# Performance work log

Hardware: AMD Instinct MI355X
Metric: run time of the kernel (lower is better)

Reference implementation:

```python
import jax, jax.numpy as jnp
import numpy as np

B, S, E, H = 4, 2048, 1024, 16
D = E // H  # head_dim = 64


def setup_inputs() -> dict:
    key = jax.random.key(0)
    ks = jax.random.split(key, 5)
    return {
        "x": jax.random.normal(ks[0], (B, S, E), dtype=jnp.float32),
        "w_qkv": jax.random.normal(ks[1], (3 * E, E), dtype=jnp.float32) * (E ** -0.5),
        "b_qkv": jax.random.normal(ks[2], (3 * E,), dtype=jnp.float32) * 0.02,
        "w_proj": jax.random.normal(ks[3], (E, E), dtype=jnp.float32) * (E ** -0.5),
        "b_proj": jax.random.normal(ks[4], (E,), dtype=jnp.float32) * 0.02,
    }


def reference(x, w_qkv, b_qkv, w_proj, b_proj):
    # fused QKV projection: [B,S,E] -> [B,S,3E] -> [B,S,3,H,D]
    qkv = (jnp.einsum("bse,fe->bsf", x, w_qkv) + b_qkv).reshape(B, S, 3, H, D)
    q, k, v = qkv[:, :, 0], qkv[:, :, 1], qkv[:, :, 2]  # each [B,S,H,D]
    scale = 1.0 / jnp.sqrt(jnp.asarray(D, dtype=q.dtype))
    scores = jnp.einsum("bqhd,bkhd->bhqk", q, k) * scale  # [B,H,S,S]
    attn = jax.nn.softmax(scores, axis=-1)
    out = jnp.einsum("bhqk,bkhd->bqhd", attn, v).reshape(B, S, E)
    return jnp.einsum("bse,fe->bsf", out, w_proj) + b_proj
```

## Files before the change

kernel.cpp:

```cpp
#include <hip/hip_runtime.h>
#include <cstdint>
#include <cstddef>

#define B_ 4
#define S_ 2048
#define E_ 1024
#define H_ 16
#define D_ 64
#define M_ (B_*S_)
#define NE_ ((size_t)B_*H_*S_*D_)

typedef unsigned int  u32;
typedef unsigned short u16;
typedef __attribute__((ext_vector_type(8))) short bf16x8;
typedef __attribute__((ext_vector_type(4))) float f32x4;
typedef __attribute__((ext_vector_type(2))) unsigned int u32x2;

__device__ __forceinline__ u16 f2bf(float x) {
    u32 u = __float_as_uint(x);
    u32 r = (u + 0x7FFFu + ((u >> 16) & 1u)) >> 16;
    return (u16)r;
}
__device__ __forceinline__ float bf2f(u16 h) { return __uint_as_float((u32)h << 16); }

__device__ __forceinline__ u32 cvtpk_bf16(float lo, float hi) {
    u32 r;
    asm("v_cvt_pk_bf16_f32 %0, %1, %2" : "=v"(r) : "v"(lo), "v"(hi));
    return r;
}

__device__ __forceinline__ void gload_lds16(const void* gsrc, void* lds) {
    __builtin_amdgcn_global_load_lds(
        (const __attribute__((address_space(1))) u32*)gsrc,
        (__attribute__((address_space(3))) u32*)lds, 16, 0, 0);
}


__global__ __launch_bounds__(256)
void convert_img(const float* __restrict__ src, u16* __restrict__ dh, u16* __restrict__ dl)
{
    const int tile = blockIdx.x;
    const int nt = tile >> 4, kt = tile & 15;
    const size_t tb = (size_t)tile << 12;
    #pragma unroll
    for (int u = 0; u < 2; ++u) {
        const int ci = threadIdx.x + u * 256;
        const int r  = ci >> 3;
        const int c  = ci & 7;
        const float* s = src + ((size_t)(nt * 64 + r)) * 1024 + kt * 64 + c * 8;
        const float4 f0 = *(const float4*)s;
        const float4 f1 = *(const float4*)(s + 4);
        const float vals[8] = {f0.x, f0.y, f0.z, f0.w, f1.x, f1.y, f1.z, f1.w};
        __align__(16) short hs[8];
        __align__(16) short ls[8];
        #pragma unroll
        for (int j = 0; j < 8; ++j) {
            const u16 h = f2bf(vals[j]);
            hs[j] = (short)h;
            ls[j] = (short)f2bf(vals[j] - bf2f(h));
        }
        const size_t eoff = tb + r * 64 + ((size_t)(c ^ (r & 7)) << 3);
        *(bf16x8*)(dh + eoff) = *(const bf16x8*)hs;
        *(bf16x8*)(dl + eoff) = *(const bf16x8*)ls;
    }
}

template<int MODE>
__global__ __launch_bounds__(256)
void gemm_mfma(const u16* __restrict__ AIh, const u16* __restrict__ AIl,
               const u16* __restrict__ BIh, const u16* __restrict__ BIl,
               const float* __restrict__ bias, float* __restrict__ Cout,
               u16* __restrict__ qh, u16* __restrict__ ql,
               u16* __restrict__ kh,
               u16* __restrict__ vh, u16* __restrict__ vl)
{
    __shared__ __align__(16) u16 sA[2][2][4096];
    __shared__ __align__(16) u16 sB[2][2][4096];

    const int tid = threadIdx.x, lane = tid & 63, w = tid >> 6;
    const int quad = lane >> 4, l15 = lane & 15;
    const int m0  = blockIdx.x * 128;
    const int n0  = blockIdx.y * 128;
    const int mt0 = blockIdx.x * 2;
    const int nt0 = blockIdx.y * 2;
    const int rw  = w >> 1;
    const int cw  = w & 1;

    const int isB = w >> 1;
    const int sbw = w & 1;

    f32x4 acc[4][4];
    #pragma unroll
    for (int i = 0; i < 4; ++i)
        #pragma unroll
        for (int j = 0; j < 4; ++j)
            acc[i][j] = (f32x4){0.f, 0.f, 0.f, 0.f};

    for (int kt = 0; kt < 16; ++kt) {
        __syncthreads();
        {
            const size_t atile = ((size_t)((mt0 + sbw) * 16 + kt)) << 12;
            const size_t btile = ((size_t)((nt0 + sbw) * 16 + kt)) << 12;
            const u16* srcH = isB ? (BIh + btile) : (AIh + atile);
            const u16* srcL = isB ? (BIl + btile) : (AIl + atile);
            u16* dstH = isB ? &sB[sbw][0][0] : &sA[sbw][0][0];
            u16* dstL = isB ? &sB[sbw][1][0] : &sA[sbw][1][0];
            #pragma unroll
            for (int it = 0; it < 8; ++it)
                gload_lds16(srcH + it * 512 + lane * 8, dstH + it * 512);
            #pragma unroll
            for (int it = 0; it < 8; ++it)
                gload_lds16(srcL + it * 512 + lane * 8, dstL + it * 512);
        }
        __syncthreads();

        #pragma unroll
        for (int kk = 0; kk < 2; ++kk) {
            bf16x8 aH[4], aL[4], bH[4], bL[4];
            #pragma unroll
            for (int i = 0; i < 4; ++i) {
                const int r = i * 16 + l15;
                const int off = r * 64 + (((kk * 4 + quad) ^ (r & 7)) << 3);
                aH[i] = *(const bf16x8*)&sA[rw][0][off];
                aL[i] = *(const bf16x8*)&sA[rw][1][off];
            }
            #pragma unroll
            for (int j = 0; j < 4; ++j) {
                const int r = j * 16 + l15;
                const int off = r * 64 + (((kk * 4 + quad) ^ (r & 7)) << 3);
                bH[j] = *(const bf16x8*)&sB[cw][0][off];
                bL[j] = *(const bf16x8*)&sB[cw][1][off];
            }
            #pragma unroll
            for (int i = 0; i < 4; ++i)
                #pragma unroll
                for (int j = 0; j < 4; ++j) {
                    acc[i][j] = __builtin_amdgcn_mfma_f32_16x16x32_bf16(aL[i], bH[j], acc[i][j], 0, 0, 0);
                    acc[i][j] = __builtin_amdgcn_mfma_f32_16x16x32_bf16(aH[i], bL[j], acc[i][j], 0, 0, 0);
                    acc[i][j] = __builtin_amdgcn_mfma_f32_16x16x32_bf16(aH[i], bH[j], acc[i][j], 0, 0, 0);
                }
        }
    }

    const int fbase = n0 + cw * 64;
    float bj[4];
    #pragma unroll
    for (int j = 0; j < 4; ++j) bj[j] = bias[fbase + j * 16 + l15];

    if (MODE == 0) {
        const int cR = fbase >> 10;
        const int hh = (fbase >> 6) & 15;
        #pragma unroll
        for (int i = 0; i < 4; ++i)
            #pragma unroll
            for (int j = 0; j < 4; ++j)
                #pragma unroll
                for (int reg = 0; reg < 4; ++reg) {
                    float val = acc[i][j][reg] + bj[j];
                    const int m = m0 + rw * 64 + i * 16 + quad * 4 + reg;
                    const int d = j * 16 + l15;
                    const int bb = m >> 11, s = m & 2047;
                    const int bh = bb * 16 + hh;
                    if (cR == 0) val *= 0.18033688011112042f;
                    const u16 h = f2bf(val);
                    if (cR == 0) {
                        const u16 lo = f2bf(val - bf2f(h));
                        const size_t idx = ((size_t)bh * 2048 + s) * 64 + d;
                        qh[idx] = h; ql[idx] = lo;
                    } else if (cR == 1) {
                        const size_t tile = (size_t)bh * 32 + (s >> 6);
                        const int r = s & 63;
                        const size_t off = (tile << 12) + r * 64 + (((d >> 3) ^ (r & 7)) << 3) + (d & 7);
                        kh[off] = h;
                    } else {
                        const u16 lo = f2bf(val - bf2f(h));
                        const size_t tile = (size_t)bh * 32 + (s >> 6);
                        const size_t off = (tile << 12) + d * 64 + ((((s & 63) >> 3) ^ (d & 7)) << 3) + (s & 7);
                        vh[off] = h; vl[off] = lo;
                    }
                }
    } else {
        #pragma unroll
        for (int i = 0; i < 4; ++i)
            #pragma unroll
            for (int j = 0; j < 4; ++j)
                #pragma unroll
                for (int reg = 0; reg < 4; ++reg) {
                    const int m = m0 + rw * 64 + i * 16 + quad * 4 + reg;
                    const int f = fbase + j * 16 + l15;
                    Cout[(size_t)m * 1024 + f] = acc[i][j][reg] + bj[j];
                }
    }
}

__global__ __launch_bounds__(256, 3)
void attn_mfma(const u16* __restrict__ qh, const u16* __restrict__ ql,
               const u16* __restrict__ kh,
               const u16* __restrict__ vh, const u16* __restrict__ vl,
               u16* __restrict__ oh, u16* __restrict__ ol)
{
    __shared__ __align__(16) u16 KV[3][4096];

    const int tid  = threadIdx.x;
    const int lane = tid & 63, w = tid >> 6;
    const int quad = lane >> 4, l15 = lane & 15;
    const int bh = blockIdx.y;
    const int q0 = blockIdx.x * 128 + w * 32;

    bf16x8 Qf[2][2][2];
    #pragma unroll
    for (int qs = 0; qs < 2; ++qs)
        #pragma unroll
        for (int kk = 0; kk < 2; ++kk) {
            const size_t idx = ((size_t)bh * S_ + q0 + qs * 16 + l15) * 64 + kk * 32 + quad * 8;
            Qf[qs][kk][0] = *(const bf16x8*)(qh + idx);
            Qf[qs][kk][1] = *(const bf16x8*)(ql + idx);
        }

    f32x4 O[2][4];
    float l_part[2] = {0.f, 0.f};
    #pragma unroll
    for (int qs = 0; qs < 2; ++qs)
        #pragma unroll
        for (int ds = 0; ds < 4; ++ds)
            O[qs][ds] = (f32x4){0.f, 0.f, 0.f, 0.f};

    const char* gk[3] = {(const char*)kh, (const char*)vh, (const char*)vl};

    for (int kt = 0; kt < S_ / 64; ++kt) {
        __syncthreads();
        const size_t tb = (((size_t)bh * 32 + kt) << 13);
        #pragma unroll
        for (int a = 0; a < 3; ++a)
            #pragma unroll
            for (int it = 0; it < 2; ++it) {
                const int off = w * 2048 + it * 1024;
                gload_lds16(gk[a] + tb + off + lane * 16, (char*)&KV[a][0] + off);
            }
        __syncthreads();

        f32x4 S[2][4];
        #pragma unroll
        for (int qs = 0; qs < 2; ++qs)
            #pragma unroll
            for (int ks = 0; ks < 4; ++ks)
                S[qs][ks] = (f32x4){-23.083120654223414f, -23.083120654223414f,
                                    -23.083120654223414f, -23.083120654223414f};

        __builtin_amdgcn_s_setprio(1);
        #pragma unroll
        for (int ks = 0; ks < 4; ++ks) {
            const int r = ks * 16 + l15;
            #pragma unroll
            for (int kk = 0; kk < 2; ++kk) {
                const int c = (kk * 4 + quad) ^ (r & 7);
                const bf16x8 Kh = *(const bf16x8*)&KV[0][r * 64 + c * 8];
                #pragma unroll
                for (int qs = 0; qs < 2; ++qs) {
                    S[qs][ks] = __builtin_amdgcn_mfma_f32_16x16x32_bf16(Kh, Qf[qs][kk][1], S[qs][ks], 0, 0, 0);
                    S[qs][ks] = __builtin_amdgcn_mfma_f32_16x16x32_bf16(Kh, Qf[qs][kk][0], S[qs][ks], 0, 0, 0);
                }
            }
        }
        __builtin_amdgcn_s_setprio(0);

        u32 PA[2][2][4];
        #pragma unroll
        for (int qs = 0; qs < 2; ++qs) {
            float lsum = 0.f;
            u32 PK[4][2];
            #pragma unroll
            for (int ks = 0; ks < 4; ++ks) {
                const float p0 = __builtin_exp2f(S[qs][ks][0]);
                const float p1 = __builtin_exp2f(S[qs][ks][1]);
                const float p2 = __builtin_exp2f(S[qs][ks][2]);
                const float p3 = __builtin_exp2f(S[qs][ks][3]);
                lsum += (p0 + p1) + (p2 + p3);
                PK[ks][0] = cvtpk_bf16(p0, p1);
                PK[ks][1] = cvtpk_bf16(p2, p3);
            }
            l_part[qs] += lsum;
            #pragma unroll
            for (int kk = 0; kk < 2; ++kk) {
                const u32x2 t0 = __builtin_amdgcn_permlane32_swap(PK[2 * kk][0], PK[2 * kk + 1][0], false, false);
                const u32x2 w02 = __builtin_amdgcn_permlane16_swap(t0.x, t0.y, false, false);
                const u32x2 t1 = __builtin_amdgcn_permlane32_swap(PK[2 * kk][1], PK[2 * kk + 1][1], false, false);
                const u32x2 w13 = __builtin_amdgcn_permlane16_swap(t1.x, t1.y, false, false);
                PA[qs][kk][0] = w02.x;
                PA[qs][kk][1] = w13.x;
                PA[qs][kk][2] = w02.y;
                PA[qs][kk][3] = w13.y;
            }
        }

        __builtin_amdgcn_s_setprio(1);
        #pragma unroll
        for (int kk = 0; kk < 2; ++kk) {
            union { u32 w4[4]; bf16x8 v; } pu0, pu1;
            #pragma unroll
            for (int c = 0; c < 4; ++c) { pu0.w4[c] = PA[0][kk][c]; pu1.w4[c] = PA[1][kk][c]; }
            const bf16x8 paf[2] = {pu0.v, pu1.v};
            #pragma unroll
            for (int ds = 0; ds < 4; ++ds) {
                const int r = ds * 16 + l15;
                const int c = (kk * 4 + quad) ^ (r & 7);
                const bf16x8 Vh = *(const bf16x8*)&KV[1][r * 64 + c * 8];
                const bf16x8 Vl = *(const bf16x8*)&KV[2][r * 64 + c * 8];
                #pragma unroll
                for (int qs = 0; qs < 2; ++qs) {
                    O[qs][ds] = __builtin_amdgcn_mfma_f32_16x16x32_bf16(Vl, paf[qs], O[qs][ds], 0, 0, 0);
                    O[qs][ds] = __builtin_amdgcn_mfma_f32_16x16x32_bf16(Vh, paf[qs], O[qs][ds], 0, 0, 0);
                }
            }
        }
        __builtin_amdgcn_s_setprio(0);
    }

    float linv[2];
    #pragma unroll
    for (int qs = 0; qs < 2; ++qs) {
        float rs = l_part[qs];
        rs += __shfl_xor(rs, 16);
        rs += __shfl_xor(rs, 32);
        linv[qs] = 1.f / rs;
    }

    const int bb = bh >> 4, hh = bh & 15;
    #pragma unroll
    for (int qs = 0; qs < 2; ++qs) {
        const float inv = linv[qs];
        const int s = q0 + qs * 16 + l15;
        const int m = bb * 2048 + s;
        const int mt = m >> 6, r = m & 63;
        const size_t tbase = ((size_t)(mt * 16 + hh)) << 12;
        #pragma unroll
        for (int ds = 0; ds < 4; ++ds) {
            const int d0 = ds * 16 + quad * 4;
            const float v0 = O[qs][ds][0] * inv;
            const float v1 = O[qs][ds][1] * inv;
            const float v2 = O[qs][ds][2] * inv;
            const float v3 = O[qs][ds][3] * inv;
            const u32 h01 = cvtpk_bf16(v0, v1);
            const u32 h23 = cvtpk_bf16(v2, v3);
            const float r0 = v0 - bf2f((u16)h01);
            const float r1 = v1 - bf2f((u16)(h01 >> 16));
            const float r2 = v2 - bf2f((u16)h23);
            const float r3 = v3 - bf2f((u16)(h23 >> 16));
            const u32 l01 = cvtpk_bf16(r0, r1);
            const u32 l23 = cvtpk_bf16(r2, r3);
            const size_t off = tbase + r * 64 + (size_t)((((d0 >> 3) ^ (r & 7)) << 3) + (d0 & 7));
            *(u32x2*)(oh + off) = (u32x2){h01, h23};
            *(u32x2*)(ol + off) = (u32x2){l01, l23};
        }
    }
}

extern "C" void kernel_launch(void* const* d_in, const int* in_sizes, int n_in,
                              void* d_out, int out_size, void* d_ws, size_t ws_size,
                              hipStream_t stream) {
    const float* x      = (const float*)d_in[0];
    const float* w_qkv  = (const float*)d_in[1];
    const float* b_qkv  = (const float*)d_in[2];
    const float* w_proj = (const float*)d_in[3];
    const float* b_proj = (const float*)d_in[4];
    float* out = (float*)d_out;

    u16* qh  = (u16*)d_ws;
    u16* ql  = qh + NE_;
    u16* kh  = ql + NE_;
    u16* vh  = kh + NE_;
    u16* vl  = vh + NE_;
    u16* xh  = vl + NE_;
    u16* xl  = xh + NE_;
    u16* wqh = xl + NE_;
    u16* wql = wqh + (size_t)3 * 1024 * 1024;
    u16* oh  = xh;
    u16* ol  = xl;
    u16* wph = wqh;
    u16* wpl = wph + (size_t)1024 * 1024;

    convert_img<<<(M_ / 64) * 16, 256, 0, stream>>>(x, xh, xl);
    convert_img<<<48 * 16, 256, 0, stream>>>(w_qkv, wqh, wql);

    {
        dim3 grid(M_ / 128, (3 * E_) / 128);
        gemm_mfma<0><<<grid, 256, 0, stream>>>(xh, xl, wqh, wql,
                                               b_qkv, nullptr, qh, ql, kh, vh, vl);
    }
    {
        dim3 grid(S_ / 128, B_ * H_);
        attn_mfma<<<grid, 256, 0, stream>>>(qh, ql, kh, vh, vl, oh, ol);
    }
    convert_img<<<16 * 16, 256, 0, stream>>>(w_proj, wph, wpl);
    {
        dim3 grid(M_ / 128, E_ / 128);
        gemm_mfma<1><<<grid, 256, 0, stream>>>(oh, ol, wph, wpl,
                                               b_proj, out, nullptr, nullptr, nullptr,
                                               nullptr, nullptr);
    }
}
```

Baseline: 438.9 us.

## Double-buffer GEMM LDS tiles with 32-wide K image layout and 256x128 blocks

Re-lays out the bf16 hi/lo image tiles as 64x32 K-slices with a new XOR swizzle, in convert_img and in the attention output writer. The GEMM now uses 512-thread blocks covering 256x128, a double-buffered LDS ring, and a prefetch of the next K-slice issued before the MFMAs, with one barrier per iteration and raised wave priority around the MFMA block. This is meant to hide global-to-LDS latency and increase B-tile reuse, at the cost of more LDS per block and a need for all layout producers and consumers to stay consistent.

```diff
diff --git a/kernel.cpp b/kernel.cpp
--- a/kernel.cpp
+++ b/kernel.cpp
@@ -40,33 +40,32 @@
 void convert_img(const float* __restrict__ src, u16* __restrict__ dh, u16* __restrict__ dl)
 {
     const int tile = blockIdx.x;
-    const int nt = tile >> 4, kt = tile & 15;
-    const size_t tb = (size_t)tile << 12;
-    #pragma unroll
-    for (int u = 0; u < 2; ++u) {
-        const int ci = threadIdx.x + u * 256;
-        const int r  = ci >> 3;
-        const int c  = ci & 7;
-        const float* s = src + ((size_t)(nt * 64 + r)) * 1024 + kt * 64 + c * 8;
-        const float4 f0 = *(const float4*)s;
-        const float4 f1 = *(const float4*)(s + 4);
-        const float vals[8] = {f0.x, f0.y, f0.z, f0.w, f1.x, f1.y, f1.z, f1.w};
-        __align__(16) short hs[8];
-        __align__(16) short ls[8];
-        #pragma unroll
-        for (int j = 0; j < 8; ++j) {
-            const u16 h = f2bf(vals[j]);
-            hs[j] = (short)h;
-            ls[j] = (short)f2bf(vals[j] - bf2f(h));
-        }
-        const size_t eoff = tb + r * 64 + ((size_t)(c ^ (r & 7)) << 3);
-        *(bf16x8*)(dh + eoff) = *(const bf16x8*)hs;
-        *(bf16x8*)(dl + eoff) = *(const bf16x8*)ls;
-    }
+    const int rt = tile >> 5, kt = tile & 31;
+    const size_t tb = (size_t)tile * 2048;
+    const int ci = threadIdx.x;
+    const int l  = ci >> 3;
+    const int ph = ci & 7;
+    const int s  = ph ^ (l & 7);
+    const int r  = (l << 1) | (s >> 2);
+    const int k0 = (s & 3) << 3;
+    const float* sp = src + ((size_t)(rt * 64 + r)) * 1024 + kt * 32 + k0;
+    const float4 f0 = *(const float4*)sp;
+    const float4 f1 = *(const float4*)(sp + 4);
+    const float vals[8] = {f0.x, f0.y, f0.z, f0.w, f1.x, f1.y, f1.z, f1.w};
+    __align__(16) short hs[8];
+    __align__(16) short ls[8];
+    #pragma unroll
+    for (int j = 0; j < 8; ++j) {
+        const u16 h = f2bf(vals[j]);
+        hs[j] = (short)h;
+        ls[j] = (short)f2bf(vals[j] - bf2f(h));
+    }
+    *(bf16x8*)(dh + tb + ci * 8) = *(const bf16x8*)hs;
+    *(bf16x8*)(dl + tb + ci * 8) = *(const bf16x8*)ls;
 }
 
 template<int MODE>
-__global__ __launch_bounds__(256)
+__global__ __launch_bounds__(512, 2)
 void gemm_mfma(const u16* __restrict__ AIh, const u16* __restrict__ AIl,
                const u16* __restrict__ BIh, const u16* __restrict__ BIl,
                const float* __restrict__ bias, float* __restrict__ Cout,
@@ -74,20 +73,26 @@
                u16* __restrict__ kh,
                u16* __restrict__ vh, u16* __restrict__ vl)
 {
-    __shared__ __align__(16) u16 sA[2][2][4096];
-    __shared__ __align__(16) u16 sB[2][2][4096];
+    __shared__ __align__(16) u16 sT[2][12][2048];
 
     const int tid = threadIdx.x, lane = tid & 63, w = tid >> 6;
     const int quad = lane >> 4, l15 = lane & 15;
-    const int m0  = blockIdx.x * 128;
+    const int m0  = blockIdx.x * 256;
     const int n0  = blockIdx.y * 128;
-    const int mt0 = blockIdx.x * 2;
+    const int mt0 = blockIdx.x * 4;
     const int nt0 = blockIdx.y * 2;
     const int rw  = w >> 1;
     const int cw  = w & 1;
 
-    const int isB = w >> 1;
-    const int sbw = w & 1;
+    const u16* srcq[6];
+    #pragma unroll
+    for (int it = 0; it < 6; ++it) {
+        const int g = w * 6 + it;
+        const int t = g >> 2, qtr = g & 3;
+        const u16* img = (t < 4) ? AIh : (t < 8) ? AIl : (t < 10) ? BIh : BIl;
+        const int rtile = (t < 8) ? (mt0 + (t & 3)) : (nt0 + (t & 1));
+        srcq[it] = img + (size_t)rtile * (32 * 2048) + qtr * 512 + lane * 8;
+    }
 
     f32x4 acc[4][4];
     #pragma unroll
@@ -96,50 +101,46 @@
         for (int j = 0; j < 4; ++j)
             acc[i][j] = (f32x4){0.f, 0.f, 0.f, 0.f};
 
-    for (int kt = 0; kt < 16; ++kt) {
+    #pragma unroll
+    for (int it = 0; it < 6; ++it)
+        gload_lds16(srcq[it], (char*)&sT[0][0][0] + (w * 6 + it) * 1024);
+    __syncthreads();
+
+    #pragma unroll 2
+    for (int kt = 0; kt < 32; ++kt) {
+        const int cur = kt & 1;
+        bf16x8 aH[4], aL[4], bH[4], bL[4];
+        #pragma unroll
+        for (int i = 0; i < 4; ++i) {
+            const int r = i * 16 + l15, l = r >> 1;
+            const int off = l * 64 + (((((r & 1) << 2) + quad) ^ (l & 7)) << 3);
+            aH[i] = *(const bf16x8*)&sT[cur][rw][off];
+            aL[i] = *(const bf16x8*)&sT[cur][4 + rw][off];
+        }
+        #pragma unroll
+        for (int j = 0; j < 4; ++j) {
+            const int r = j * 16 + l15, l = r >> 1;
+            const int off = l * 64 + (((((r & 1) << 2) + quad) ^ (l & 7)) << 3);
+            bH[j] = *(const bf16x8*)&sT[cur][8 + cw][off];
+            bL[j] = *(const bf16x8*)&sT[cur][10 + cw][off];
+        }
+        if (kt < 31) {
+            #pragma unroll
+            for (int it = 0; it < 6; ++it)
+                gload_lds16(srcq[it] + (size_t)(kt + 1) * 2048,
+                            (char*)&sT[cur ^ 1][0][0] + (w * 6 + it) * 1024);
+        }
+        __builtin_amdgcn_s_setprio(1);
+        #pragma unroll
+        for (int i = 0; i < 4; ++i)
+            #pragma unroll
+            for (int j = 0; j < 4; ++j) {
+                acc[i][j] = __builtin_amdgcn_mfma_f32_16x16x32_bf16(aL[i], bH[j], acc[i][j], 0, 0, 0);
+                acc[i][j] = __builtin_amdgcn_mfma_f32_16x16x32_bf16(aH[i], bL[j], acc[i][j], 0, 0, 0);
+                acc[i][j] = __builtin_amdgcn_mfma_f32_16x16x32_bf16(aH[i], bH[j], acc[i][j], 0, 0, 0);
+            }
+        __builtin_amdgcn_s_setprio(0);
         __syncthreads();
-        {
-            const size_t atile = ((size_t)((mt0 + sbw) * 16 + kt)) << 12;
-            const size_t btile = ((size_t)((nt0 + sbw) * 16 + kt)) << 12;
-            const u16* srcH = isB ? (BIh + btile) : (AIh + atile);
-            const u16* srcL = isB ? (BIl + btile) : (AIl + atile);
-            u16* dstH = isB ? &sB[sbw][0][0] : &sA[sbw][0][0];
-            u16* dstL = isB ? &sB[sbw][1][0] : &sA[sbw][1][0];
-            #pragma unroll
-            for (int it = 0; it < 8; ++it)
-                gload_lds16(srcH + it * 512 + lane * 8, dstH + it * 512);
-            #pragma unroll
-            for (int it = 0; it < 8; ++it)
-                gload_lds16(srcL + it * 512 + lane * 8, dstL + it * 512);
-        }
-        __syncthreads();
-
-        #pragma unroll
-        for (int kk = 0; kk < 2; ++kk) {
-            bf16x8 aH[4], aL[4], bH[4], bL[4];
-            #pragma unroll
-            for (int i = 0; i < 4; ++i) {
-                const int r = i * 16 + l15;
-                const int off = r * 64 + (((kk * 4 + quad) ^ (r & 7)) << 3);
-                aH[i] = *(const bf16x8*)&sA[rw][0][off];
-                aL[i] = *(const bf16x8*)&sA[rw][1][off];
-            }
-            #pragma unroll
-            for (int j = 0; j < 4; ++j) {
-                const int r = j * 16 + l15;
-                const int off = r * 64 + (((kk * 4 + quad) ^ (r & 7)) << 3);
-                bH[j] = *(const bf16x8*)&sB[cw][0][off];
-                bL[j] = *(const bf16x8*)&sB[cw][1][off];
-            }
-            #pragma unroll
-            for (int i = 0; i < 4; ++i)
-                #pragma unroll
-                for (int j = 0; j < 4; ++j) {
-                    acc[i][j] = __builtin_amdgcn_mfma_f32_16x16x32_bf16(aL[i], bH[j], acc[i][j], 0, 0, 0);
-                    acc[i][j] = __builtin_amdgcn_mfma_f32_16x16x32_bf16(aH[i], bL[j], acc[i][j], 0, 0, 0);
-                    acc[i][j] = __builtin_amdgcn_mfma_f32_16x16x32_bf16(aH[i], bH[j], acc[i][j], 0, 0, 0);
-                }
-        }
     }
 
     const int fbase = n0 + cw * 64;
@@ -332,7 +333,8 @@
         const int s = q0 + qs * 16 + l15;
         const int m = bb * 2048 + s;
         const int mt = m >> 6, r = m & 63;
-        const size_t tbase = ((size_t)(mt * 16 + hh)) << 12;
+        const int l = r >> 1;
+        const size_t tb0 = ((size_t)(mt * 32 + hh * 2)) * 2048;
         #pragma unroll
         for (int ds = 0; ds < 4; ++ds) {
             const int d0 = ds * 16 + quad * 4;
@@ -348,7 +350,9 @@
             const float r3 = v3 - bf2f((u16)(h23 >> 16));
             const u32 l01 = cvtpk_bf16(r0, r1);
             const u32 l23 = cvtpk_bf16(r2, r3);
-            const size_t off = tbase + r * 64 + (size_t)((((d0 >> 3) ^ (r & 7)) << 3) + (d0 & 7));
+            const int c  = (d0 & 31) >> 3;
+            const int ph = (((r & 1) << 2) + c) ^ (l & 7);
+            const size_t off = tb0 + (size_t)(d0 >> 5) * 2048 + l * 64 + ph * 8 + (d0 & 7);
             *(u32x2*)(oh + off) = (u32x2){h01, h23};
             *(u32x2*)(ol + off) = (u32x2){l01, l23};
         }
@@ -379,22 +383,22 @@
     u16* wph = wqh;
     u16* wpl = wph + (size_t)1024 * 1024;
 
-    convert_img<<<(M_ / 64) * 16, 256, 0, stream>>>(x, xh, xl);
-    convert_img<<<48 * 16, 256, 0, stream>>>(w_qkv, wqh, wql);
+    convert_img<<<128 * 32, 256, 0, stream>>>(x, xh, xl);
+    convert_img<<<48 * 32, 256, 0, stream>>>(w_qkv, wqh, wql);
 
     {
-        dim3 grid(M_ / 128, (3 * E_) / 128);
-        gemm_mfma<0><<<grid, 256, 0, stream>>>(xh, xl, wqh, wql,
+        dim3 grid(M_ / 256, (3 * E_) / 128);
+        gemm_mfma<0><<<grid, 512, 0, stream>>>(xh, xl, wqh, wql,
                                                b_qkv, nullptr, qh, ql, kh, vh, vl);
     }
     {
         dim3 grid(S_ / 128, B_ * H_);
         attn_mfma<<<grid, 256, 0, stream>>>(qh, ql, kh, vh, vl, oh, ol);
     }
-    convert_img<<<16 * 16, 256, 0, stream>>>(w_proj, wph, wpl);
+    convert_img<<<16 * 32, 256, 0, stream>>>(w_proj, wph, wpl);
     {
-        dim3 grid(M_ / 128, E_ / 128);
-        gemm_mfma<1><<<grid, 256, 0, stream>>>(oh, ol, wph, wpl,
+        dim3 grid(M_ / 256, E_ / 128);
+        gemm_mfma<1><<<grid, 512, 0, stream>>>(oh, ol, wph, wpl,
                                                b_proj, out, nullptr, nullptr, nullptr,
                                                nullptr, nullptr);
     }
```

Measured after the change: 429.9 us. -2.1%, faster.
